# Kernel optimization log

Hardware: AMD Instinct MI355X
Metric: run time of the kernel (lower is better)

Reference implementation:

```python
import jax, jax.numpy as jnp
import numpy as np
import math

B = 32
TS_LEN = 8192
DSEG = 32
S = TS_LEN // DSEG          # 256 segments
DM = 256                    # dim_model
NBITS = 8                   # bits of the bucket signature (synthetic _compute_index)
NBUCKETS = 2 ** NBITS       # 256 ragged-vocab buckets, made uniform here
W = 512                     # words per bucket (uniform -> vocabulary_dist[b] = b*W)
NHAAR = 6                   # min(log2(S)=8, max_haar_depth=6)
LMAX = 13                   # full haar depth of wavedec on length-8192 signal


def _layer_norm(x, eps=1e-5):
    m = x.mean(-1, keepdims=True)
    v = ((x - m) ** 2).mean(-1, keepdims=True)
    return (x - m) / jnp.sqrt(v + eps)


def _pos_emb():
    # sinusoidal positional embedding, matches the torch buffer construction
    pos = jnp.arange(S, dtype=jnp.float32)[:, None]
    div = jnp.exp(jnp.arange(0, DM, 2, dtype=jnp.float32) * (-math.log(10000.0) / DM))
    pe = jnp.zeros((S, DM), jnp.float32)
    pe = pe.at[:, 0::2].set(jnp.sin(pos * div))
    pe = pe.at[:, 1::2].set(jnp.cos(pos * div))
    return pe


def setup_inputs() -> dict:
    key = jax.random.key(0)
    k1, k2, k3, k4 = jax.random.split(key, 4)
    x = jax.random.normal(k1, (B, TS_LEN), jnp.float32)
    # candidate words live in [0,1] (they are compared against min-max-normalized segments)
    vocab_table = jax.random.uniform(k2, (NBUCKETS, W, DSEG), dtype=jnp.float32)
    word_emb = jax.random.normal(k3, (NBUCKETS * W, DM), jnp.float32)
    haar_emb = jax.random.normal(k4, (NHAAR + 1, DM), jnp.float32)
    return {"x": x, "vocab_table": vocab_table, "word_emb": word_emb, "haar_emb": haar_emb}


def reference(x, vocab_table, word_emb, haar_emb):
    # ---- _adjust: input length == ts_len -> identity, att_mask all ones ----
    att_mask = jnp.ones((B, S), jnp.int32)

    # ---- compute_word_embedding (vectorized over batch and segments) ----
    segs = x.reshape(B, S, DSEG)
    smin = segs.min(-1, keepdims=True)
    smax = segs.max(-1, keepdims=True)
    seg_norm = (segs - smin) / (smax - smin + 1e-8)
    # synthetic _compute_index: 8-bit signature (chunk mean above segment mean)
    chunk_means = segs.reshape(B, S, NBITS, DSEG // NBITS).mean(-1)       # [B,S,8]
    bits = (chunk_means > segs.mean(-1, keepdims=True)).astype(jnp.int32)
    bucket = (bits * (2 ** jnp.arange(NBITS, dtype=jnp.int32))).sum(-1)   # [B,S]
    cand = vocab_table[bucket]                                            # [B,S,W,DSEG]
    dist = jnp.abs(cand - seg_norm[:, :, None, :]).sum(-1)                # [B,S,W] L1 cdist
    best = jnp.argmin(dist, axis=-1)                                      # [B,S]
    word_embed = word_emb[bucket * W + best]                              # [B,S,DM]

    # ---- compute_haar_embedding (pywt.wavedec with 'haar', first NHAAR+1 coeffs) ----
    a = x
    details = []
    sqrt2 = jnp.float32(math.sqrt(2.0))
    for _ in range(LMAX):
        even = a[:, 0::2]
        odd = a[:, 1::2]
        details.append((even - odd) / sqrt2)
        a = (even + odd) / sqrt2
    coeffs = [a] + details[::-1]                # [cA_L, cD_L, ..., cD_1]
    taken = coeffs[: NHAAR + 1]
    rows = [jnp.repeat(c, S // c.shape[1], axis=1) for c in taken]        # each [B,S]
    haar_matrix = jnp.stack(rows, axis=-1)                                # [B,S,NHAAR+1]
    haar_matrix = haar_matrix * att_mask[..., None].astype(haar_matrix.dtype)
    haar_embed = haar_matrix @ haar_emb                                   # [B,S,DM]
    haar_embed = _layer_norm(haar_embed)

    out = word_embed + haar_embed + _pos_emb()
    out = _layer_norm(out)
    return (out, att_mask)
```

## Files before the change

### kernel.cpp

```cpp
#include <hip/hip_runtime.h>
#include <math.h>

#define BB 32
#define TS 8192
#define DSEG 32
#define SS 256
#define DM 256
#define W 512
#define CAP 1024

__global__ __launch_bounds__(256) void prep_haar_kernel(
    const float* __restrict__ x,
    float* __restrict__ segn_g,
    unsigned char* __restrict__ bucketc,
    unsigned long long* __restrict__ bestkey,
    float* __restrict__ hout)
{
    const int blk = blockIdx.x;
    const int t = threadIdx.x;

    if (blk < 1024) {
        const int segBase = blk * 8;
        __shared__ float sseg[8][32];
        sseg[t >> 5][t & 31] = x[(size_t)segBase * 32 + t];
        __syncthreads();

        const int hw = t >> 5;
        const int h = hw & 1;
        const int l = t & 31;
        const int seg = segBase + hw;

        float v = sseg[hw][l];
        float mn = v, mx = v, sm = v;
#pragma unroll
        for (int m = 1; m <= 16; m <<= 1) {
            mn = fminf(mn, __shfl_xor(mn, m));
            mx = fmaxf(mx, __shfl_xor(mx, m));
            sm += __shfl_xor(sm, m);
        }
        float mean = sm * (1.0f / 32.0f);
        float cm = 0.0f;
        if (l < 8) {
            cm = ((sseg[hw][4 * l] + sseg[hw][4 * l + 1]) + sseg[hw][4 * l + 2]) +
                 sseg[hw][4 * l + 3];
            cm *= 0.25f;
        }
        unsigned long long bal = __ballot(l < 8 && cm > mean);
        segn_g[(size_t)seg * 32 + l] = (v - mn) / (mx - mn + 1e-8f);
        if (l == 0) bucketc[seg] = (unsigned char)((bal >> (h * 32)) & 0xFF);
        if (l == 1) bestkey[seg] = ~0ULL;
    } else {
        const int b = blk - 1024;
        const int lane = t;
        if (lane >= 64) return;
        const float* xb = x + (size_t)b * TS + (size_t)lane * 128;
        const float is2 = 0.70710678118654752440f;

        float a[64];
#pragma unroll
        for (int i = 0; i < 32; ++i) {
            float4 u = *(const float4*)(xb + 4 * i);
            a[2 * i + 0] = (u.x + u.y) * is2;
            a[2 * i + 1] = (u.z + u.w) * is2;
        }
#pragma unroll
        for (int len = 64; len > 1; len >>= 1) {
#pragma unroll
            for (int j = 0; j < (len >> 1); ++j)
                a[j] = (a[2 * j] + a[2 * j + 1]) * is2;
        }
        float val = a[0];
        float* ob = hout + b * 64;
#pragma unroll
        for (int len = 64; len > 1; len >>= 1) {
            float e = __shfl(val, 2 * lane);
            float o = __shfl(val, 2 * lane + 1);
            int half = len >> 1;
            if (lane < half) {
                ob[half + lane] = (e - o) * is2;
                val = (e + o) * is2;
            }
        }
        if (lane == 0) ob[0] = val;
    }
}

__global__ __launch_bounds__(512) void search_kernel(
    const float* __restrict__ vocab,
    const float* __restrict__ segn_g,
    const unsigned char* __restrict__ bucketc,
    unsigned long long* __restrict__ bestkey)
{
    const int bucket = blockIdx.x >> 1;
    const int half = blockIdx.x & 1;
    const int t = threadIdx.x;
    const int lane = t & 63;
    const int wid = t >> 6;

    __shared__ float vsh[256 * 32];
    __shared__ int list[CAP];
    __shared__ int cnt;
    if (t == 0) cnt = 0;
    __syncthreads();

    for (int i = t; i < BB * SS; i += 512) {
        if (bucketc[i] == (unsigned char)bucket) {
            int p = atomicAdd(&cnt, 1);
            if (p < CAP) list[p] = i;
        }
    }

    const float* vb = vocab + ((size_t)bucket * W + (size_t)half * 256) * DSEG;
#pragma unroll 2
    for (int f = t; f < 2048; f += 512) {
        int r = f >> 3, q = f & 7;
        float4 u = ((const float4*)vb)[f];
        int sq = q ^ (r & 7);
        *(float4*)&vsh[r * 32 + sq * 4] = u;
    }
    __syncthreads();

    int n = cnt; if (n > CAP) n = CAP;
    for (int i = wid; i < n; i += 8) {
        const int seg = list[i];
        const float* sp = segn_g + (size_t)seg * 32;
        float sv[32];
#pragma unroll
        for (int d = 0; d < 32; ++d) sv[d] = sp[d];

        unsigned long long best = ~0ULL;
#pragma unroll
        for (int c = 0; c < 4; ++c) {
            const int r = c * 64 + lane;
            float dist = 0.0f;
#pragma unroll
            for (int q = 0; q < 8; ++q) {
                float4 u = *(const float4*)&vsh[r * 32 + ((q ^ (r & 7)) * 4)];
                dist += fabsf(u.x - sv[4 * q + 0]);
                dist += fabsf(u.y - sv[4 * q + 1]);
                dist += fabsf(u.z - sv[4 * q + 2]);
                dist += fabsf(u.w - sv[4 * q + 3]);
            }
            unsigned w = (unsigned)(half * 256 + r);
            unsigned long long key =
                ((unsigned long long)__float_as_uint(dist) << 32) | w;
            if (key < best) best = key;
        }
#pragma unroll
        for (int m = 1; m < 64; m <<= 1) {
            unsigned long long o = __shfl_xor(best, m);
            if (o < best) best = o;
        }
        if (lane == 0) atomicMin(bestkey + seg, best);
    }
}

__global__ __launch_bounds__(256) void out_kernel(
    const float* __restrict__ wemb,
    const float* __restrict__ hemb,
    const float* __restrict__ hcoef,
    const unsigned char* __restrict__ bucketc,
    const unsigned long long* __restrict__ bestkey,
    float* __restrict__ out)
{
    const int bs = (blockIdx.x << 2) + (threadIdx.x >> 6);
    const int lane = threadIdx.x & 63;
    const int b = bs >> 8;
    const int s = bs & 255;

    const int bucket = bucketc[bs];
    const int bestw = (int)(unsigned)(bestkey[bs] & 0xFFFFFFFFull);

    const float* hb = hcoef + b * 64;
    float hk[7];
    hk[0] = hb[0];
#pragma unroll
    for (int k = 1; k <= 6; ++k)
        hk[k] = hb[(1 << (k - 1)) + (s >> (8 - (k - 1)))];

    float h0 = 0.f, h1 = 0.f, h2 = 0.f, h3 = 0.f;
#pragma unroll
    for (int k = 0; k < 7; ++k) {
        float4 he = ((const float4*)(hemb + k * DM))[lane];
        h0 += hk[k] * he.x; h1 += hk[k] * he.y;
        h2 += hk[k] * he.z; h3 += hk[k] * he.w;
    }

    float sm = ((h0 + h1) + h2) + h3;
    float sq = ((h0 * h0 + h1 * h1) + h2 * h2) + h3 * h3;
#pragma unroll
    for (int m = 1; m < 64; m <<= 1) {
        sm += __shfl_xor(sm, m);
        sq += __shfl_xor(sq, m);
    }
    float mh = sm * (1.0f / 256.0f);
    float vh = fmaxf(sq * (1.0f / 256.0f) - mh * mh, 0.0f);
    float rs = 1.0f / sqrtf(vh + 1e-5f);
    float n0 = (h0 - mh) * rs, n1 = (h1 - mh) * rs;
    float n2 = (h2 - mh) * rs, n3 = (h3 - mh) * rs;

    const size_t row = (size_t)bucket * W + (size_t)bestw;
    float4 wv = ((const float4*)(wemb + row * DM))[lane];

    const float cexp = -9.210340371976184f / 256.0f;
    float dva = expf((float)(4 * lane) * cexp);
    float dvb = expf((float)(4 * lane + 2) * cexp);
    float anga = (float)s * dva, angb = (float)s * dvb;
    float o0 = wv.x + n0 + sinf(anga);
    float o1 = wv.y + n1 + cosf(anga);
    float o2 = wv.z + n2 + sinf(angb);
    float o3 = wv.w + n3 + cosf(angb);

    float sm2 = ((o0 + o1) + o2) + o3;
    float sq2 = ((o0 * o0 + o1 * o1) + o2 * o2) + o3 * o3;
#pragma unroll
    for (int m = 1; m < 64; m <<= 1) {
        sm2 += __shfl_xor(sm2, m);
        sq2 += __shfl_xor(sq2, m);
    }
    float mo = sm2 * (1.0f / 256.0f);
    float vo = fmaxf(sq2 * (1.0f / 256.0f) - mo * mo, 0.0f);
    float rs2 = 1.0f / sqrtf(vo + 1e-5f);

    float4 res;
    res.x = (o0 - mo) * rs2; res.y = (o1 - mo) * rs2;
    res.z = (o2 - mo) * rs2; res.w = (o3 - mo) * rs2;
    ((float4*)(out + (size_t)bs * DM))[lane] = res;
    if (lane == 0) out[(size_t)BB * SS * DM + bs] = 1.0f;
}

extern "C" void kernel_launch(void* const* d_in, const int* in_sizes, int n_in,
                              void* d_out, int out_size, void* d_ws, size_t ws_size,
                              hipStream_t stream) {
    const float* x     = (const float*)d_in[0];
    const float* vocab = (const float*)d_in[1];
    const float* wemb  = (const float*)d_in[2];
    const float* hemb  = (const float*)d_in[3];
    float* out = (float*)d_out;

    char* ws = (char*)d_ws;
    float* segn                  = (float*)ws;
    unsigned long long* bestkey  = (unsigned long long*)(ws + 1048576);
    unsigned char* bucketc       = (unsigned char*)(ws + 1048576 + 65536);
    float* hco                   = (float*)(ws + 1048576 + 65536 + 8192);

    prep_haar_kernel<<<1056, 256, 0, stream>>>(x, segn, bucketc, bestkey, hco);
    search_kernel<<<512, 512, 0, stream>>>(vocab, segn, bucketc, bestkey);
    out_kernel<<<2048, 256, 0, stream>>>(wemb, hemb, hco, bucketc, bestkey, out);
}
```

Measured before the change: 214.6 us.

## Precompute positional table, vectorize bucket scan, process two segments per wave

Adds 256 blocks to the prep kernel that build the sinusoidal positional table once into workspace, so the output kernel reads it instead of evaluating exp/sin/cos per element. The search kernel now scans the bucket array with one 16-byte load per thread instead of a strided byte loop. Each wave also computes L1 distances for two segments per shared-memory vocab load, which halves LDS traffic per segment but doubles register use for the segment vectors. Waves whose last segment has no partner recompute a duplicate segment and skip its atomic update.

Result: faster. 206.9 us (-3.6%).

```diff
diff --git a/kernel.cpp b/kernel.cpp
--- a/kernel.cpp
+++ b/kernel.cpp
@@ -9,12 +9,13 @@
 #define W 512
 #define CAP 1024
 
-__global__ __launch_bounds__(256) void prep_haar_kernel(
+__global__ __launch_bounds__(256) void prep_haar_pe_kernel(
     const float* __restrict__ x,
     float* __restrict__ segn_g,
     unsigned char* __restrict__ bucketc,
     unsigned long long* __restrict__ bestkey,
-    float* __restrict__ hout)
+    float* __restrict__ hout,
+    float* __restrict__ pe_g)
 {
     const int blk = blockIdx.x;
     const int t = threadIdx.x;
@@ -49,7 +50,7 @@
         segn_g[(size_t)seg * 32 + l] = (v - mn) / (mx - mn + 1e-8f);
         if (l == 0) bucketc[seg] = (unsigned char)((bal >> (h * 32)) & 0xFF);
         if (l == 1) bestkey[seg] = ~0ULL;
-    } else {
+    } else if (blk < 1056) {
         const int b = blk - 1024;
         const int lane = t;
         if (lane >= 64) return;
@@ -82,6 +83,12 @@
             }
         }
         if (lane == 0) ob[0] = val;
+    } else {
+        const int s = blk - 1056;
+        const float cexp = -9.210340371976184f / 256.0f;
+        float dv = expf((float)(t & ~1) * cexp);
+        float ang = (float)s * dv;
+        pe_g[s * DM + t] = (t & 1) ? cosf(ang) : sinf(ang);
     }
 }
 
@@ -103,10 +110,16 @@
     if (t == 0) cnt = 0;
     __syncthreads();
 
-    for (int i = t; i < BB * SS; i += 512) {
-        if (bucketc[i] == (unsigned char)bucket) {
-            int p = atomicAdd(&cnt, 1);
-            if (p < CAP) list[p] = i;
+    {
+        uint4 v16 = ((const uint4*)bucketc)[t];
+        const unsigned char* pb = (const unsigned char*)&v16;
+        int base = t * 16;
+#pragma unroll
+        for (int j = 0; j < 16; ++j) {
+            if (pb[j] == (unsigned char)bucket) {
+                int p = atomicAdd(&cnt, 1);
+                if (p < CAP) list[p] = base + j;
+            }
         }
     }
 
@@ -121,37 +134,52 @@
     __syncthreads();
 
     int n = cnt; if (n > CAP) n = CAP;
-    for (int i = wid; i < n; i += 8) {
-        const int seg = list[i];
-        const float* sp = segn_g + (size_t)seg * 32;
-        float sv[32];
-#pragma unroll
-        for (int d = 0; d < 32; ++d) sv[d] = sp[d];
-
-        unsigned long long best = ~0ULL;
+    for (int i = 2 * wid; i < n; i += 16) {
+        const int segA = list[i];
+        const bool hasB = (i + 1 < n);
+        const int segB = hasB ? list[i + 1] : segA;
+        const float* spA = segn_g + (size_t)segA * 32;
+        const float* spB = segn_g + (size_t)segB * 32;
+        float svA[32], svB[32];
+#pragma unroll
+        for (int d = 0; d < 32; ++d) { svA[d] = spA[d]; svB[d] = spB[d]; }
+
+        unsigned long long bestA = ~0ULL, bestB = ~0ULL;
 #pragma unroll
         for (int c = 0; c < 4; ++c) {
             const int r = c * 64 + lane;
-            float dist = 0.0f;
+            float dA = 0.0f, dB = 0.0f;
 #pragma unroll
             for (int q = 0; q < 8; ++q) {
                 float4 u = *(const float4*)&vsh[r * 32 + ((q ^ (r & 7)) * 4)];
-                dist += fabsf(u.x - sv[4 * q + 0]);
-                dist += fabsf(u.y - sv[4 * q + 1]);
-                dist += fabsf(u.z - sv[4 * q + 2]);
-                dist += fabsf(u.w - sv[4 * q + 3]);
+                dA += fabsf(u.x - svA[4 * q + 0]);
+                dA += fabsf(u.y - svA[4 * q + 1]);
+                dA += fabsf(u.z - svA[4 * q + 2]);
+                dA += fabsf(u.w - svA[4 * q + 3]);
+                dB += fabsf(u.x - svB[4 * q + 0]);
+                dB += fabsf(u.y - svB[4 * q + 1]);
+                dB += fabsf(u.z - svB[4 * q + 2]);
+                dB += fabsf(u.w - svB[4 * q + 3]);
             }
             unsigned w = (unsigned)(half * 256 + r);
-            unsigned long long key =
-                ((unsigned long long)__float_as_uint(dist) << 32) | w;
-            if (key < best) best = key;
+            unsigned long long kA =
+                ((unsigned long long)__float_as_uint(dA) << 32) | w;
+            unsigned long long kB =
+                ((unsigned long long)__float_as_uint(dB) << 32) | w;
+            if (kA < bestA) bestA = kA;
+            if (kB < bestB) bestB = kB;
         }
 #pragma unroll
         for (int m = 1; m < 64; m <<= 1) {
-            unsigned long long o = __shfl_xor(best, m);
-            if (o < best) best = o;
-        }
-        if (lane == 0) atomicMin(bestkey + seg, best);
+            unsigned long long oA = __shfl_xor(bestA, m);
+            unsigned long long oB = __shfl_xor(bestB, m);
+            if (oA < bestA) bestA = oA;
+            if (oB < bestB) bestB = oB;
+        }
+        if (lane == 0) {
+            atomicMin(bestkey + segA, bestA);
+            if (hasB) atomicMin(bestkey + segB, bestB);
+        }
     }
 }
 
@@ -159,6 +187,7 @@
     const float* __restrict__ wemb,
     const float* __restrict__ hemb,
     const float* __restrict__ hcoef,
+    const float* __restrict__ pe_g,
     const unsigned char* __restrict__ bucketc,
     const unsigned long long* __restrict__ bestkey,
     float* __restrict__ out)
@@ -202,14 +231,12 @@
     const size_t row = (size_t)bucket * W + (size_t)bestw;
     float4 wv = ((const float4*)(wemb + row * DM))[lane];
 
-    const float cexp = -9.210340371976184f / 256.0f;
-    float dva = expf((float)(4 * lane) * cexp);
-    float dvb = expf((float)(4 * lane + 2) * cexp);
-    float anga = (float)s * dva, angb = (float)s * dvb;
-    float o0 = wv.x + n0 + sinf(anga);
-    float o1 = wv.y + n1 + cosf(anga);
-    float o2 = wv.z + n2 + sinf(angb);
-    float o3 = wv.w + n3 + cosf(angb);
+    float4 pv = ((const float4*)(pe_g + s * DM))[lane];
+
+    float o0 = wv.x + n0 + pv.x;
+    float o1 = wv.y + n1 + pv.y;
+    float o2 = wv.z + n2 + pv.z;
+    float o3 = wv.w + n3 + pv.w;
 
     float sm2 = ((o0 + o1) + o2) + o3;
     float sq2 = ((o0 * o0 + o1 * o1) + o2 * o2) + o3 * o3;
@@ -243,8 +270,11 @@
     unsigned long long* bestkey  = (unsigned long long*)(ws + 1048576);
     unsigned char* bucketc       = (unsigned char*)(ws + 1048576 + 65536);
     float* hco                   = (float*)(ws + 1048576 + 65536 + 8192);
-
-    prep_haar_kernel<<<1056, 256, 0, stream>>>(x, segn, bucketc, bestkey, hco);
+    float* pe_g                  = (float*)(ws + 1048576 + 65536 + 16384);
+
+    prep_haar_pe_kernel<<<1312, 256, 0, stream>>>(x, segn, bucketc, bestkey,
+                                                  hco, pe_g);
     search_kernel<<<512, 512, 0, stream>>>(vocab, segn, bucketc, bestkey);
-    out_kernel<<<2048, 256, 0, stream>>>(wemb, hemb, hco, bucketc, bestkey, out);
-}
+    out_kernel<<<2048, 256, 0, stream>>>(wemb, hemb, hco, pe_g, bucketc,
+                                         bestkey, out);
+}
```
